# Kernel optimization log

Measured on AMD Instinct MI355X. Metric: run time of the kernel, lower is better.

The kernel has to match this reference:

```python
import jax, jax.numpy as jnp
import numpy as np

MARGIN = 0.3
BIG = 1e5  # same constant the torch code uses to mask out same-id entries for the min


def setup_inputs() -> dict:
    key = jax.random.key(0)
    k1, k2, k3 = jax.random.split(key, 3)
    B, D, N_LUT, N_ID = 4096, 1024, 5000, 1024
    feat = jax.random.normal(k1, (B, D), dtype=jnp.float32)
    lut = jax.random.normal(k2, (N_LUT, D), dtype=jnp.float32)
    id = jax.random.randint(k3, (B,), 0, N_ID, dtype=jnp.int64)
    return {"feat": feat, "lut": lut, "id": id}


def reference(feat, lut, id):
    # feat_oim = lut[id]  (gather rows of the OIM lookup table)
    feat_oim = lut[id]  # (B, D)

    # Pairwise euclidean distance dist[i,j] = sqrt(||feat_i - feat_oim_j||^2 + 1e-12)
    # via the dot-product trick (avoids materializing the (B,B,D) diff tensor).
    sq_a = jnp.sum(feat * feat, axis=1)          # (B,)
    sq_b = jnp.sum(feat_oim * feat_oim, axis=1)  # (B,)
    sq = sq_a[:, None] + sq_b[None, :] - 2.0 * (feat @ feat_oim.T)  # (B, B)
    dist = jnp.sqrt(jnp.maximum(sq, 0.0) + 1e-12)

    # Masks (mode='id'):
    same_id = id[:, None] == id[None, :]               # (B, B) bool
    eye = jnp.eye(feat.shape[0], dtype=bool)
    positive_mask = same_id & ~eye

    # Batch-hard mining (n_dis=0):
    max_positive = jnp.max(dist * positive_mask.astype(dist.dtype), axis=1)   # hardest positive
    min_negative = jnp.min(dist + BIG * same_id.astype(dist.dtype), axis=1)   # hardest negative
    z = max_positive - min_negative

    # float margin path: hinge
    b_loss = jnp.maximum(z + MARGIN, 0.0)  # (B,)
    return b_loss
```

## Files before the change

kernel.cpp:

```cpp
#include <hip/hip_runtime.h>
#include <hip/hip_bf16.h>

#define B_N    4096
#define D_K    1024
#define N_C    1024
#define MARGIN 0.3f

typedef __attribute__((ext_vector_type(8))) short short8;
typedef __attribute__((ext_vector_type(4))) float f32x4;

__device__ inline ushort f2bf(float f) {
    unsigned u = __float_as_uint(f);
    unsigned r = (u + 0x7fffu + ((u >> 16) & 1u)) >> 16;
    return (ushort)r;
}

__device__ inline void async16(const ushort* g, ushort* l) {
    __builtin_amdgcn_global_load_lds(
        (const __attribute__((address_space(1))) void*)g,
        (__attribute__((address_space(3))) void*)l,
        16, 0, 0);
}

__global__ void prep_all(const float* __restrict__ feat,
                         const float* __restrict__ lut,
                         const int* __restrict__ id,
                         ushort* __restrict__ featP, ushort* __restrict__ lutB,
                         float* __restrict__ sq_a, float* __restrict__ sq_b,
                         int* __restrict__ cnt,
                         int* __restrict__ maxb, int* __restrict__ minb) {
    int b = blockIdx.x;
    int t = threadIdx.x;

    if (b == B_N + N_C) {
        __shared__ int hc[N_C];
        #pragma unroll
        for (int i = 0; i < 4; i++) hc[t * 4 + i] = 0;
        __syncthreads();
        #pragma unroll
        for (int i = 0; i < 16; i++) atomicAdd(&hc[id[t * 16 + i]], 1);
        __syncthreads();
        #pragma unroll
        for (int i = 0; i < 4; i++) cnt[t * 4 + i] = hc[t * 4 + i];
        return;
    }

    if (b < 16) {
        int i = b * 256 + t;
        maxb[i] = 0;
        minb[i] = 0x7F800000;
    }
    const float* src; float* sq;
    if (b < B_N) { src = feat + (size_t)b * D_K;          sq = sq_a + b; }
    else         { src = lut + (size_t)(b - B_N) * D_K;   sq = sq_b + (b - B_N); }

    float4 v = ((const float4*)src)[t];
    float ss = v.x * v.x + v.y * v.y + v.z * v.z + v.w * v.w;
    ushort4 bb;
    bb.x = f2bf(v.x); bb.y = f2bf(v.y); bb.z = f2bf(v.z); bb.w = f2bf(v.w);

    if (b < B_N) {
        int g = b >> 4, rl = b & 15;
        int kt = t >> 3, h = (t >> 1) & 3, e0 = (t & 1) * 4;
        size_t off = ((size_t)g * 32 + kt) * 512 + (rl + h * 16) * 8 + e0;
        *(ushort4*)(featP + off) = bb;
    } else {
        ((ushort4*)(lutB + (size_t)(b - B_N) * D_K))[t] = bb;
    }

    int lane = t & 63, w = t >> 6;
    #pragma unroll
    for (int o = 1; o < 64; o <<= 1) ss += __shfl_xor(ss, o);
    __shared__ float red[4];
    if (lane == 0) red[w] = ss;
    __syncthreads();
    if (t == 0) *sq = red[0] + red[1] + red[2] + red[3];
}

__global__ __launch_bounds__(256, 4)
void dist_kernel(const ushort* __restrict__ Ap, const ushort* __restrict__ Bm,
                 const float* __restrict__ sqa, const float* __restrict__ sqb,
                 const int* __restrict__ ids, const int* __restrict__ cnt,
                 int* __restrict__ maxb, int* __restrict__ minb) {
    __shared__ __align__(16) ushort lB[2][2048];

    const int t = threadIdx.x;
    const int lane = t & 63;
    const int wid = t >> 6;
    const int l15 = lane & 15;
    const int h = lane >> 4;

    const int bid = blockIdx.y * gridDim.x + blockIdx.x;
    const int swz = (bid & 7) * 64 + (bid >> 3);
    const int rb = swz >> 4, cb = swz & 15;

    int p = t * 8;
    int rp = p >> 6;
    int sl = ((p >> 3) & 7) ^ (rp & 7);
    int rr = rp * 2 + (sl >> 2);
    int jj = sl & 3;
    const ushort* gB = Bm + (size_t)(cb * 64 + rr) * D_K + jj * 8;
    const int wo = wid * 512;

    const int par = (l15 & 1) << 2;
    int offB[4];
    #pragma unroll
    for (int nf = 0; nf < 4; nf++) {
        int line = (l15 >> 1) + nf * 8;
        offB[nf] = line * 64 + (((par | h) ^ (line & 7)) << 3);
    }

    const ushort* pa0 = Ap + ((size_t)(rb * 8 + wid * 2 + 0) * 32) * 512 + lane * 8;
    const ushort* pa1 = Ap + ((size_t)(rb * 8 + wid * 2 + 1) * 32) * 512 + lane * 8;

    f32x4 acc[2][4] = {};
    short8 aE0, aE1, aO0, aO1, bfv[4];

    async16(gB, &lB[0][0] + wo);
    aE0 = *(const short8*)(pa0);
    aE1 = *(const short8*)(pa1);

#define MFMA16(av0, av1)                                                    \
    _Pragma("unroll") for (int nf = 0; nf < 4; nf++) {                      \
        acc[0][nf] = __builtin_amdgcn_mfma_f32_16x16x32_bf16(               \
            av0, bfv[nf], acc[0][nf], 0, 0, 0);                             \
        acc[1][nf] = __builtin_amdgcn_mfma_f32_16x16x32_bf16(               \
            av1, bfv[nf], acc[1][nf], 0, 0, 0);                             \
    }

#define ITER(KT, C0, C1, N0, N1)                                            \
    {                                                                       \
        const int s_ = (KT) & 1;                                            \
        if ((KT) < 31) {                                                    \
            async16(gB + ((KT) + 1) * 32, &lB[s_ ^ 1][0] + wo);             \
            N0 = *(const short8*)(pa0 + ((KT) + 1) * 512);                  \
            N1 = *(const short8*)(pa1 + ((KT) + 1) * 512);                  \
            __builtin_amdgcn_sched_barrier(0);                              \
            asm volatile("s_waitcnt vmcnt(5)" ::: "memory");                \
        } else {                                                            \
            asm volatile("s_waitcnt vmcnt(0)" ::: "memory");                \
        }                                                                   \
        __builtin_amdgcn_sched_barrier(0);                                  \
        __builtin_amdgcn_s_barrier();               \
        __builtin_amdgcn_sched_barrier(0);                                  \
        _Pragma("unroll") for (int nf = 0; nf < 4; nf++)                    \
            bfv[nf] = *(const short8*)(&lB[s_][0] + offB[nf]);              \
        MFMA16(C0, C1);                                                     \
        __builtin_amdgcn_sched_barrier(0);                                  \
        __builtin_amdgcn_s_barrier();                \
    }

    for (int kt = 0; kt < 32; kt += 2) {
        ITER(kt,     aE0, aE1, aO0, aO1);
        ITER(kt + 1, aO0, aO1, aE0, aE1);
    }
#undef ITER
#undef MFMA16

    int colg[4]; float sb2[4]; int c2[4];
    #pragma unroll
    for (int nf = 0; nf < 4; nf++) {
        int c = cb * 64 + nf * 16 + l15;
        colg[nf] = c; sb2[nf] = sqb[c]; c2[nf] = cnt[c];
    }
    #pragma unroll
    for (int m = 0; m < 2; m++) {
        #pragma unroll
        for (int r = 0; r < 4; r++) {
            int row = rb * 128 + wid * 32 + m * 16 + h * 4 + r;
            float sa = sqa[row];
            int ida = ids[row];
            float mx = 0.0f, mn = 3.0e38f;
            #pragma unroll
            for (int nf = 0; nf < 4; nf++) {
                float s2 = sa + sb2[nf] - 2.0f * acc[m][nf][r];
                float d = sqrtf(fmaxf(s2, 0.0f) + 1e-12f);
                bool iseq = (colg[nf] == ida);
                float pv = (iseq && c2[nf] >= 2) ? d : 0.0f;
                float nv = (c2[nf] > 0 && !iseq) ? d : 3.0e38f;
                mx = fmaxf(mx, pv);
                mn = fminf(mn, nv);
            }
            #pragma unroll
            for (int o = 1; o < 16; o <<= 1) {
                mx = fmaxf(mx, __shfl_xor(mx, o));
                mn = fminf(mn, __shfl_xor(mn, o));
            }
            if (l15 == 0) {
                atomicMax(maxb + row, __float_as_int(mx));
                atomicMin(minb + row, __float_as_int(mn));
            }
        }
    }
}

__global__ void finalize_k(const int* __restrict__ maxb, const int* __restrict__ minb,
                           float* __restrict__ out) {
    int i = blockIdx.x * blockDim.x + threadIdx.x;
    if (i < B_N) {
        float z = __int_as_float(maxb[i]) - __int_as_float(minb[i]) + MARGIN;
        out[i] = fmaxf(z, 0.0f);
    }
}

extern "C" void kernel_launch(void* const* d_in, const int* in_sizes, int n_in,
                              void* d_out, int out_size, void* d_ws, size_t ws_size,
                              hipStream_t stream) {
    const float* feat = (const float*)d_in[0];
    const float* lut  = (const float*)d_in[1];
    const int*   id   = (const int*)d_in[2];
    float* out = (float*)d_out;

    char* ws = (char*)d_ws;
    ushort* featP = (ushort*)ws;
    ushort* lutB  = (ushort*)(ws + (size_t)B_N * D_K * 2);
    float*  sq_a  = (float*)(ws + (size_t)(B_N + N_C) * D_K * 2);
    float*  sq_b  = sq_a + B_N;
    int*    cnt   = (int*)(sq_b + N_C);
    int*    maxb  = cnt + N_C;
    int*    minb  = maxb + B_N;

    prep_all<<<B_N + N_C + 1, 256, 0, stream>>>(feat, lut, id, featP, lutB,
                                                sq_a, sq_b, cnt, maxb, minb);

    dim3 grid(N_C / 64, B_N / 128);
    dist_kernel<<<grid, 256, 0, stream>>>(featP, lutB, sq_a, sq_b, id, cnt,
                                          maxb, minb);

    finalize_k<<<16, 256, 0, stream>>>(maxb, minb, out);
}
```

Before: 38.81 us.

## Load pre-packed MFMA fragments directly into registers with larger per-wave tiles

```diff
diff --git a/kernel.cpp b/kernel.cpp
--- a/kernel.cpp
+++ b/kernel.cpp
@@ -15,17 +15,17 @@
     return (ushort)r;
 }
 
-__device__ inline void async16(const ushort* g, ushort* l) {
-    __builtin_amdgcn_global_load_lds(
-        (const __attribute__((address_space(1))) void*)g,
-        (__attribute__((address_space(3))) void*)l,
-        16, 0, 0);
+__device__ inline size_t packOff(int row, int t) {
+    int g = row >> 6, mf = (row >> 4) & 3, l15 = row & 15;
+    int kt = t >> 4, ks = (t >> 3) & 1, h = (t >> 1) & 3, e0 = (t & 1) * 4;
+    return ((size_t)(g * 16 + kt) * 8 + mf * 2 + ks) * 512
+         + (h * 16 + l15) * 8 + e0;
 }
 
 __global__ void prep_all(const float* __restrict__ feat,
                          const float* __restrict__ lut,
                          const int* __restrict__ id,
-                         ushort* __restrict__ featP, ushort* __restrict__ lutB,
+                         ushort* __restrict__ featP, ushort* __restrict__ lutP,
                          float* __restrict__ sq_a, float* __restrict__ sq_b,
                          int* __restrict__ cnt,
                          int* __restrict__ maxb, int* __restrict__ minb) {
@@ -50,23 +50,21 @@
         maxb[i] = 0;
         minb[i] = 0x7F800000;
     }
-    const float* src; float* sq;
-    if (b < B_N) { src = feat + (size_t)b * D_K;          sq = sq_a + b; }
-    else         { src = lut + (size_t)(b - B_N) * D_K;   sq = sq_b + (b - B_N); }
-
+    const float* src; ushort* dstP; float* sq; int row;
+    if (b < B_N) {
+        row = b;
+        src = feat + (size_t)row * D_K;
+        dstP = featP; sq = sq_a + row;
+    } else {
+        row = b - B_N;
+        src = lut + (size_t)row * D_K;
+        dstP = lutP; sq = sq_b + row;
+    }
     float4 v = ((const float4*)src)[t];
     float ss = v.x * v.x + v.y * v.y + v.z * v.z + v.w * v.w;
     ushort4 bb;
     bb.x = f2bf(v.x); bb.y = f2bf(v.y); bb.z = f2bf(v.z); bb.w = f2bf(v.w);
-
-    if (b < B_N) {
-        int g = b >> 4, rl = b & 15;
-        int kt = t >> 3, h = (t >> 1) & 3, e0 = (t & 1) * 4;
-        size_t off = ((size_t)g * 32 + kt) * 512 + (rl + h * 16) * 8 + e0;
-        *(ushort4*)(featP + off) = bb;
-    } else {
-        ((ushort4*)(lutB + (size_t)(b - B_N) * D_K))[t] = bb;
-    }
+    *(ushort4*)(dstP + packOff(row, t)) = bb;
 
     int lane = t & 63, w = t >> 6;
     #pragma unroll
@@ -77,13 +75,11 @@
     if (t == 0) *sq = red[0] + red[1] + red[2] + red[3];
 }
 
-__global__ __launch_bounds__(256, 4)
-void dist_kernel(const ushort* __restrict__ Ap, const ushort* __restrict__ Bm,
+__global__ __launch_bounds__(256, 2)
+void dist_kernel(const ushort* __restrict__ Ap, const ushort* __restrict__ Bp,
                  const float* __restrict__ sqa, const float* __restrict__ sqb,
                  const int* __restrict__ ids, const int* __restrict__ cnt,
                  int* __restrict__ maxb, int* __restrict__ minb) {
-    __shared__ __align__(16) ushort lB[2][2048];
-
     const int t = threadIdx.x;
     const int lane = t & 63;
     const int wid = t >> 6;
@@ -91,71 +87,40 @@
     const int h = lane >> 4;
 
     const int bid = blockIdx.y * gridDim.x + blockIdx.x;
-    const int swz = (bid & 7) * 64 + (bid >> 3);
+    const int swz = (bid & 7) * 32 + (bid >> 3);
     const int rb = swz >> 4, cb = swz & 15;
 
-    int p = t * 8;
-    int rp = p >> 6;
-    int sl = ((p >> 3) & 7) ^ (rp & 7);
-    int rr = rp * 2 + (sl >> 2);
-    int jj = sl & 3;
-    const ushort* gB = Bm + (size_t)(cb * 64 + rr) * D_K + jj * 8;
-    const int wo = wid * 512;
+    const ushort* aBase = Ap + (size_t)(rb * 4 + wid) * 65536 + lane * 8;
+    const ushort* bBase = Bp + (size_t)cb * 65536 + lane * 8;
 
-    const int par = (l15 & 1) << 2;
-    int offB[4];
-    #pragma unroll
-    for (int nf = 0; nf < 4; nf++) {
-        int line = (l15 >> 1) + nf * 8;
-        offB[nf] = line * 64 + (((par | h) ^ (line & 7)) << 3);
+    f32x4 acc[4][4] = {};
+    short8 aR0[8], bR0[8], aR1[8], bR1[8];
+
+#define LD(AS, BS, KT)                                                      \
+    _Pragma("unroll") for (int f = 0; f < 8; f++) {                         \
+        AS[f] = *(const short8*)(aBase + (KT) * 4096 + f * 512);            \
+        BS[f] = *(const short8*)(bBase + (KT) * 4096 + f * 512);            \
     }
 
-    const ushort* pa0 = Ap + ((size_t)(rb * 8 + wid * 2 + 0) * 32) * 512 + lane * 8;
-    const ushort* pa1 = Ap + ((size_t)(rb * 8 + wid * 2 + 1) * 32) * 512 + lane * 8;
+#define MM(AS, BS)                                                          \
+    __builtin_amdgcn_s_setprio(1);                                          \
+    _Pragma("unroll") for (int mf = 0; mf < 4; mf++)                        \
+    _Pragma("unroll") for (int nf = 0; nf < 4; nf++)                        \
+    _Pragma("unroll") for (int ks = 0; ks < 2; ks++)                        \
+        acc[mf][nf] = __builtin_amdgcn_mfma_f32_16x16x32_bf16(              \
+            AS[mf * 2 + ks], BS[nf * 2 + ks], acc[mf][nf], 0, 0, 0);        \
+    __builtin_amdgcn_s_setprio(0);
 
-    f32x4 acc[2][4] = {};
-    short8 aE0, aE1, aO0, aO1, bfv[4];
-
-    async16(gB, &lB[0][0] + wo);
-    aE0 = *(const short8*)(pa0);
-    aE1 = *(const short8*)(pa1);
-
-#define MFMA16(av0, av1)                                                    \
-    _Pragma("unroll") for (int nf = 0; nf < 4; nf++) {                      \
-        acc[0][nf] = __builtin_amdgcn_mfma_f32_16x16x32_bf16(               \
-            av0, bfv[nf], acc[0][nf], 0, 0, 0);                             \
-        acc[1][nf] = __builtin_amdgcn_mfma_f32_16x16x32_bf16(               \
-            av1, bfv[nf], acc[1][nf], 0, 0, 0);                             \
+    LD(aR0, bR0, 0);
+    #pragma unroll
+    for (int kt = 0; kt < 16; kt += 2) {
+        if (kt + 1 < 16) LD(aR1, bR1, kt + 1);
+        MM(aR0, bR0);
+        if (kt + 2 < 16) LD(aR0, bR0, kt + 2);
+        MM(aR1, bR1);
     }
-
-#define ITER(KT, C0, C1, N0, N1)                                            \
-    {                                                                       \
-        const int s_ = (KT) & 1;                                            \
-        if ((KT) < 31) {                                                    \
-            async16(gB + ((KT) + 1) * 32, &lB[s_ ^ 1][0] + wo);             \
-            N0 = *(const short8*)(pa0 + ((KT) + 1) * 512);                  \
-            N1 = *(const short8*)(pa1 + ((KT) + 1) * 512);                  \
-            __builtin_amdgcn_sched_barrier(0);                              \
-            asm volatile("s_waitcnt vmcnt(5)" ::: "memory");                \
-        } else {                                                            \
-            asm volatile("s_waitcnt vmcnt(0)" ::: "memory");                \
-        }                                                                   \
-        __builtin_amdgcn_sched_barrier(0);                                  \
-        __builtin_amdgcn_s_barrier();               \
-        __builtin_amdgcn_sched_barrier(0);                                  \
-        _Pragma("unroll") for (int nf = 0; nf < 4; nf++)                    \
-            bfv[nf] = *(const short8*)(&lB[s_][0] + offB[nf]);              \
-        MFMA16(C0, C1);                                                     \
-        __builtin_amdgcn_sched_barrier(0);                                  \
-        __builtin_amdgcn_s_barrier();                \
-    }
-
-    for (int kt = 0; kt < 32; kt += 2) {
-        ITER(kt,     aE0, aE1, aO0, aO1);
-        ITER(kt + 1, aO0, aO1, aE0, aE1);
-    }
-#undef ITER
-#undef MFMA16
+#undef LD
+#undef MM
 
     int colg[4]; float sb2[4]; int c2[4];
     #pragma unroll
@@ -164,16 +129,16 @@
         colg[nf] = c; sb2[nf] = sqb[c]; c2[nf] = cnt[c];
     }
     #pragma unroll
-    for (int m = 0; m < 2; m++) {
+    for (int mf = 0; mf < 4; mf++) {
         #pragma unroll
         for (int r = 0; r < 4; r++) {
-            int row = rb * 128 + wid * 32 + m * 16 + h * 4 + r;
+            int row = rb * 256 + wid * 64 + mf * 16 + h * 4 + r;
             float sa = sqa[row];
             int ida = ids[row];
             float mx = 0.0f, mn = 3.0e38f;
             #pragma unroll
             for (int nf = 0; nf < 4; nf++) {
-                float s2 = sa + sb2[nf] - 2.0f * acc[m][nf][r];
+                float s2 = sa + sb2[nf] - 2.0f * acc[mf][nf][r];
                 float d = sqrtf(fmaxf(s2, 0.0f) + 1e-12f);
                 bool iseq = (colg[nf] == ida);
                 float pv = (iseq && c2[nf] >= 2) ? d : 0.0f;
@@ -213,18 +178,18 @@
 
     char* ws = (char*)d_ws;
     ushort* featP = (ushort*)ws;
-    ushort* lutB  = (ushort*)(ws + (size_t)B_N * D_K * 2);
+    ushort* lutP  = (ushort*)(ws + (size_t)B_N * D_K * 2);
     float*  sq_a  = (float*)(ws + (size_t)(B_N + N_C) * D_K * 2);
     float*  sq_b  = sq_a + B_N;
     int*    cnt   = (int*)(sq_b + N_C);
     int*    maxb  = cnt + N_C;
     int*    minb  = maxb + B_N;
 
-    prep_all<<<B_N + N_C + 1, 256, 0, stream>>>(feat, lut, id, featP, lutB,
+    prep_all<<<B_N + N_C + 1, 256, 0, stream>>>(feat, lut, id, featP, lutP,
                                                 sq_a, sq_b, cnt, maxb, minb);
 
-    dim3 grid(N_C / 64, B_N / 128);
-    dist_kernel<<<grid, 256, 0, stream>>>(featP, lutB, sq_a, sq_b, id, cnt,
+    dim3 grid(16, 16);
+    dist_kernel<<<grid, 256, 0, stream>>>(featP, lutP, sq_a, sq_b, id, cnt,
                                           maxb, minb);
 
     finalize_k<<<16, 256, 0, stream>>>(maxb, minb, out);
```

New measurement: 40.57 us. 4.5% more time.
